# Performance work log

Measured on AMD Instinct MI355X. Metric: run time of the kernel, lower is better.

Reference implementation:

```python
import jax, jax.numpy as jnp
import numpy as np

B, S, V, E, H, NL, DFF = 16, 16, 64, 64, 8, 4, 2048
L = S * V
DH = E // H
NUM_GRIDS = 100
POI_DIM = 8
OV_DIM = 8


def setup_inputs() -> dict:
    key = jax.random.key(0)
    ks = jax.random.split(key, 32)
    sc = 0.05
    inp = {}
    inp['features'] = jax.random.normal(ks[0], (B, S, V, 3), jnp.float32)
    inp['overlap_tag'] = jax.random.randint(ks[1], (B, S, V), 0, 3)
    inp['poi_id'] = jax.random.randint(ks[2], (B, S, V), 0, NUM_GRIDS + 1)
    # embedders
    inp['W_raw'] = jax.random.normal(ks[3], (3, E), jnp.float32) * sc
    inp['b_raw'] = jnp.zeros((E,), jnp.float32)
    inp['pos_tab'] = jax.random.normal(ks[4], (S, E), jnp.float32) * sc
    inp['type_tab'] = jax.random.normal(ks[5], (V, E), jnp.float32) * sc
    inp['poi_tab'] = jax.random.normal(ks[6], (NUM_GRIDS + 1, POI_DIM), jnp.float32) * sc
    inp['overlap_tab'] = jax.random.normal(ks[7], (3, OV_DIM), jnp.float32) * sc
    inp['W_comb'] = jax.random.normal(ks[8], (E + OV_DIM + POI_DIM, E), jnp.float32) * sc
    inp['b_comb'] = jnp.zeros((E,), jnp.float32)
    # transformer layers (stacked over NL)
    inp['Wqkv'] = jax.random.normal(ks[9], (NL, E, 3 * E), jnp.float32) * sc
    inp['bqkv'] = jnp.zeros((NL, 3 * E), jnp.float32)
    inp['Wo'] = jax.random.normal(ks[10], (NL, E, E), jnp.float32) * sc
    inp['bo'] = jnp.zeros((NL, E), jnp.float32)
    inp['ln1_s'] = jnp.ones((NL, E), jnp.float32)
    inp['ln1_b'] = jnp.zeros((NL, E), jnp.float32)
    inp['W1'] = jax.random.normal(ks[11], (NL, E, DFF), jnp.float32) * sc
    inp['b1'] = jnp.zeros((NL, DFF), jnp.float32)
    inp['W2'] = jax.random.normal(ks[12], (NL, DFF, E), jnp.float32) * sc
    inp['b2'] = jnp.zeros((NL, E), jnp.float32)
    inp['ln2_s'] = jnp.ones((NL, E), jnp.float32)
    inp['ln2_b'] = jnp.zeros((NL, E), jnp.float32)
    inp['W_head'] = jax.random.normal(ks[13], (E, 3), jnp.float32) * sc
    inp['b_head'] = jnp.zeros((3,), jnp.float32)
    return inp


def _layer_norm(x, s, b):
    m = x.mean(-1, keepdims=True)
    v = ((x - m) ** 2).mean(-1, keepdims=True)
    return (x - m) / jnp.sqrt(v + 1e-5) * s + b


def _forward(features, overlap_tag, poi_id, W_raw, b_raw, pos_tab, type_tab,
             poi_tab, overlap_tab, W_comb, b_comb, Wqkv, bqkv, Wo, bo,
             ln1_s, ln1_b, W1, b1, W2, b2, ln2_s, ln2_b, W_head, b_head):
    # padding_idx=0 rows are zero (as in nn.Embedding(padding_idx=0))
    poi_tab = poi_tab.at[0].set(0.0)
    overlap_tab = overlap_tab.at[0].set(0.0)

    zero_mask = (features.sum(-1) == 0).reshape(B, L)  # [B, L]
    ov_idx = jnp.maximum(overlap_tag, 0)
    poi_idx = jnp.maximum(poi_id, 0)

    feat_e = features @ W_raw + b_raw                    # [B,S,V,E]
    concat = jnp.concatenate([feat_e, overlap_tab[ov_idx], poi_tab[poi_idx]], axis=-1)
    x = (concat @ W_comb + b_comb).reshape(B, L, E)      # [B,L,E]

    t_idx = jnp.repeat(jnp.arange(S), V)                 # [L]
    v_idx = jnp.tile(jnp.arange(V), S)                   # [L]
    struct_mask = (t_idx[:, None] != t_idx[None, :]) & (v_idx[:, None] != v_idx[None, :])
    full_mask = struct_mask[None] | zero_mask[:, None, :] | zero_mask[:, :, None]  # [B,L,L]
    bias = jnp.where(full_mask, -jnp.inf, 0.0)[:, None, :, :]  # [B,1,L,L]

    x = x + pos_tab[t_idx][None] + type_tab[v_idx][None]

    scale = 1.0 / jnp.sqrt(jnp.asarray(DH, x.dtype))
    for l in range(NL):
        qkv = x @ Wqkv[l] + bqkv[l]                      # [B,L,3E]
        q, k, v = jnp.split(qkv, 3, axis=-1)
        q = q.reshape(B, L, H, DH)
        k = k.reshape(B, L, H, DH)
        v = v.reshape(B, L, H, DH)
        scores = jnp.einsum('bqhd,bkhd->bhqk', q, k) * scale + bias
        attn = jax.nn.softmax(scores, axis=-1)
        o = jnp.einsum('bhqk,bkhd->bqhd', attn, v).reshape(B, L, E)
        x = _layer_norm(x + o @ Wo[l] + bo[l], ln1_s[l], ln1_b[l])
        ff = jax.nn.relu(x @ W1[l] + b1[l]) @ W2[l] + b2[l]
        x = _layer_norm(x + ff, ln2_s[l], ln2_b[l])

    last = x.reshape(B, S, V, E)[:, -1]                  # [B,V,E]
    return last @ W_head + b_head                        # [B,V,3]


def reference(features, overlap_tag, poi_id, W_raw, b_raw, pos_tab, type_tab,
              poi_tab, overlap_tab, W_comb, b_comb, Wqkv, bqkv, Wo, bo,
              ln1_s, ln1_b, W1, b1, W2, b2, ln2_s, ln2_b, W_head, b_head):
    return _forward(features, overlap_tag, poi_id, W_raw, b_raw, pos_tab, type_tab,
                    poi_tab, overlap_tab, W_comb, b_comb, Wqkv, bqkv, Wo, bo,
                    ln1_s, ln1_b, W1, b1, W2, b2, ln2_s, ln2_b, W_head, b_head)
```

## Files before the change

kernel.cpp:

```cpp
#include <hip/hip_runtime.h>
#include <math.h>

#define BB 16
#define SS 16
#define VVV 64
#define EE 64
#define HHH 8
#define NLAYER 4
#define DFF_ 2048
#define LL 1024
#define BL 16384
#define PERL 131072

typedef __attribute__((ext_vector_type(8))) _Float16 half8;
typedef __attribute__((ext_vector_type(4))) _Float16 half4v;
typedef __attribute__((ext_vector_type(2))) _Float16 half2v;
typedef __attribute__((ext_vector_type(4))) float f32x4;

#if defined(__has_builtin)
#if __has_builtin(__builtin_amdgcn_fdot2)
#define HAVE_FDOT2 1
#endif
#endif

#define SW64(m, k)  (((m) << 6) + ((((k) >> 3) ^ ((m) & 7)) << 3) + ((k) & 7))


__global__ __launch_bounds__(256) void k_prep(
    const float* __restrict__ W1, const float* __restrict__ W2,
    const float* __restrict__ Wqkv, const float* __restrict__ Wo,
    const float* __restrict__ Wcomb,
    _Float16* __restrict__ w1f, _Float16* __restrict__ w2f,
    _Float16* __restrict__ wqkvf, _Float16* __restrict__ wof,
    _Float16* __restrict__ wcombt)
{
  __shared__ float t[64 * 65];
  int bx = blockIdx.x;
  int cc = threadIdx.x & 63, rr = threadIdx.x >> 6;

  if (bx >= 272) {
    int r0 = (bx - 272) * 64;
#pragma unroll
    for (int i = 0; i < 16; i++) {
      int r = i * 4 + rr;
      if (r0 + r < 80) t[r * 65 + cc] = Wcomb[(size_t)(r0 + r) * 64 + cc];
    }
    __syncthreads();
#pragma unroll
    for (int i = 0; i < 16; i++) {
      int c = i * 4 + rr;
      if (r0 + c < 80) wcombt[(size_t)cc * 80 + r0 + c] = (_Float16)t[c * 65 + cc];
    }
    return;
  }

  const float* src; _Float16* dst; int astr;
  if (bx < 128) {
    int l = bx >> 5, g = bx & 31;
    src = W1 + (size_t)l * PERL + g * 64; astr = 2048;
    dst = w1f + (size_t)(l * 32 + g) * 4096;
  } else if (bx < 256) {
    int j = bx - 128; int l = j >> 5, g = j & 31;
    src = W2 + (size_t)l * PERL + (size_t)g * 64 * 64; astr = 64;
    dst = w2f + (size_t)(l * 32 + g) * 4096;
  } else if (bx < 268) {
    int j = bx - 256; int l = j / 3, g = j % 3;
    src = Wqkv + (size_t)l * 64 * 192 + g * 64; astr = 192;
    dst = wqkvf + (size_t)(l * 3 + g) * 4096;
  } else {
    int l = bx - 268;
    src = Wo + (size_t)l * 4096; astr = 64;
    dst = wof + (size_t)l * 4096;
  }
#pragma unroll
  for (int i = 0; i < 16; i++) {
    int a = i * 4 + rr;
    t[cc * 65 + a] = src[(size_t)a * astr + cc];
  }
  __syncthreads();
#pragma unroll
  for (int it = 0; it < 2; it++) {
    int c = threadIdx.x + it * 256;
    int frag = c >> 6, lane = c & 63;
    int m = (frag >> 1) * 16 + (lane & 15);
    int k0 = (frag & 1) * 32 + (lane >> 4) * 8;
    const float* tr = &t[m * 65 + k0];
    half8 h;
#pragma unroll
    for (int j = 0; j < 8; j++) h[j] = (_Float16)tr[j];
    *(half8*)&dst[(size_t)c * 8] = h;
  }
}

__device__ __forceinline__ void qkv_nb(
    const half8 (&af)[2][2], const _Float16* __restrict__ wqkvf,
    const float* __restrict__ bqkv, _Float16* __restrict__ qbuf,
    _Float16* __restrict__ kbuf, _Float16* __restrict__ vbuf,
    int bx, int nb, int wm, int wn, int lane)
{
  int quad = lane >> 4, l15 = lane & 15;
  const _Float16* bt = wqkvf + (size_t)nb * 4096;
  half8 bf[2][2];
#pragma unroll
  for (int nt = 0; nt < 2; nt++)
#pragma unroll
    for (int ks = 0; ks < 2; ks++)
      bf[nt][ks] = *(const half8*)&bt[(size_t)(((wn * 2 + nt) * 2 + ks) * 512) +
                                      lane * 8];
  f32x4 acc[2][2];
#pragma unroll
  for (int mt = 0; mt < 2; mt++)
#pragma unroll
    for (int nt = 0; nt < 2; nt++) {
      float bv = bqkv[nb * 64 + wn * 32 + nt * 16 + l15];
      acc[mt][nt] = (f32x4){bv, bv, bv, bv};
    }
#pragma unroll
  for (int ks = 0; ks < 2; ks++)
#pragma unroll
    for (int mt = 0; mt < 2; mt++)
#pragma unroll
      for (int nt = 0; nt < 2; nt++)
        acc[mt][nt] = __builtin_amdgcn_mfma_f32_16x16x32_f16(
            af[mt][ks], bf[nt][ks], acc[mt][nt], 0, 0, 0);
  _Float16* dst = (nb == 0) ? qbuf : ((nb == 1) ? kbuf : vbuf);
#pragma unroll
  for (int mt = 0; mt < 2; mt++)
#pragma unroll
    for (int nt = 0; nt < 2; nt++) {
      int col = wn * 32 + nt * 16 + l15;
      int h = col >> 3, d = col & 7;
#pragma unroll
      for (int r = 0; r < 4; r++) {
        int row = bx * 64 + wm * 32 + mt * 16 + quad * 4 + r;
        int b = row >> 10, rb = row & 1023;
        dst[((size_t)(b * 8 + h) * 1024 + rb) * 8 + d] = (_Float16)acc[mt][nt][r];
      }
    }
}

__device__ __forceinline__ void ffn_load(
    const _Float16* __restrict__ w1f, const _Float16* __restrict__ w2f, int g,
    half8 (&a1)[2][2], half8 (&b2w)[2][2], int wm, int wn, int lane)
{
  const _Float16* w1t_ = w1f + (size_t)g * 4096;
  const _Float16* w2t_ = w2f + (size_t)g * 4096;
#pragma unroll
  for (int ht = 0; ht < 2; ht++)
#pragma unroll
    for (int ks = 0; ks < 2; ks++)
      a1[ht][ks] = *(const half8*)&w1t_[(size_t)(((wm * 2 + ht) * 2 + ks) * 512) +
                                        lane * 8];
#pragma unroll
  for (int nt = 0; nt < 2; nt++)
#pragma unroll
    for (int ks = 0; ks < 2; ks++)
      b2w[nt][ks] = *(const half8*)&w2t_[(size_t)(((wn * 2 + nt) * 2 + ks) * 512) +
                                         lane * 8];
}

__device__ __forceinline__ void ffn_step(
    const half8 (&a1)[2][2], const half8 (&b2w)[2][2], const half8 (&xb)[2][2],
    _Float16* hsbuf, const float* __restrict__ b1, int g, f32x4 (&acc)[2][2],
    int wm, int wn, int lane)
{
  int quad = lane >> 4, l15 = lane & 15;
  f32x4 hacc[2][2];
#pragma unroll
  for (int ht = 0; ht < 2; ht++)
#pragma unroll
    for (int mt = 0; mt < 2; mt++) hacc[ht][mt] = (f32x4){0.f, 0.f, 0.f, 0.f};
#pragma unroll
  for (int ks = 0; ks < 2; ks++)
#pragma unroll
    for (int ht = 0; ht < 2; ht++)
#pragma unroll
      for (int mt = 0; mt < 2; mt++)
        hacc[ht][mt] = __builtin_amdgcn_mfma_f32_16x16x32_f16(
            a1[ht][ks], xb[mt][ks], hacc[ht][mt], 0, 0, 0);
#pragma unroll
  for (int ht = 0; ht < 2; ht++) {
    float4 bb = *(const float4*)&b1[g * 64 + wm * 32 + ht * 16 + quad * 4];
#pragma unroll
    for (int mt = 0; mt < 2; mt++) {
      f32x4 hv = hacc[ht][mt];
      half4v hp = (half4v){
          (_Float16)fmaxf(hv[0] + bb.x, 0.f), (_Float16)fmaxf(hv[1] + bb.y, 0.f),
          (_Float16)fmaxf(hv[2] + bb.z, 0.f), (_Float16)fmaxf(hv[3] + bb.w, 0.f)};
      *(half4v*)&hsbuf[SW64(wn * 32 + mt * 16 + l15,
                            wm * 32 + ht * 16 + quad * 4)] = hp;
    }
  }
  __syncthreads();
#pragma unroll
  for (int ks = 0; ks < 2; ks++)
#pragma unroll
    for (int mt = 0; mt < 2; mt++) {
      half8 a2 = *(const half8*)&hsbuf[SW64(wm * 32 + mt * 16 + l15,
                                            ks * 32 + quad * 8)];
#pragma unroll
      for (int nt = 0; nt < 2; nt++)
        acc[mt][nt] = __builtin_amdgcn_mfma_f32_16x16x32_f16(a2, b2w[nt][ks],
                                                             acc[mt][nt], 0, 0, 0);
    }
}

__global__ __launch_bounds__(256) void k_embqkv(
    const float* __restrict__ features, const int* __restrict__ ovtag,
    const int* __restrict__ poiid, const float* __restrict__ W_raw,
    const float* __restrict__ b_raw, const float* __restrict__ ov_tab,
    const float* __restrict__ poi_tab, const _Float16* __restrict__ wcombt,
    const float* __restrict__ b_comb, const float* __restrict__ pos_tab,
    const float* __restrict__ type_tab, float* __restrict__ x1,
    float* __restrict__ zm, const _Float16* __restrict__ wqkvf,
    const float* __restrict__ bqkv, _Float16* __restrict__ qbuf,
    _Float16* __restrict__ kbuf, _Float16* __restrict__ vbuf)
{
  constexpr int KP = 104;
  __shared__ _Float16 As[64 * KP];
  __shared__ _Float16 Bs[64 * KP];
  __shared__ _Float16 xs[4096];
  int tid = threadIdx.x;
  int bx = blockIdx.x;
  int m0 = bx * 64;
  int wave = tid >> 6, lane = tid & 63, quad = lane >> 4, l15 = lane & 15;
  int wm = wave >> 1, wn = wave & 1;
  for (int p = tid; p < 1536; p += 256) {
    int r = p / 24, s = p - r * 24; int c = s * 4;
    int row = m0 + r;
    float f0 = features[row * 3 + 0];
    float f1 = features[row * 3 + 1];
    float f2 = features[row * 3 + 2];
    if (s == 0) zm[row] = ((f0 + f1 + f2) == 0.f) ? 1.f : 0.f;
    half4v h;
#pragma unroll
    for (int j = 0; j < 4; j++) {
      int cc = c + j; float v;
      if (cc < 64) {
        v = b_raw[cc] + f0 * W_raw[cc] + f1 * W_raw[64 + cc] + f2 * W_raw[128 + cc];
      } else if (cc < 72) {
        int tt = ovtag[row]; v = (tt <= 0) ? 0.f : ov_tab[tt * 8 + cc - 64];
      } else if (cc < 80) {
        int tt = poiid[row]; v = (tt <= 0) ? 0.f : poi_tab[tt * 8 + cc - 72];
      } else v = 0.f;
      h[j] = (_Float16)v;
    }
    *(half4v*)&As[r * KP + c] = h;
  }
  for (int p = tid; p < 1536; p += 256) {
    int r = p / 24, s = p - r * 24; int c = s * 4;
    half4v h = (half4v){0, 0, 0, 0};
    if (c < 80) h = *(const half4v*)&wcombt[r * 80 + c];
    *(half4v*)&Bs[r * KP + c] = h;
  }
  __syncthreads();
  f32x4 acc[2][2];
#pragma unroll
  for (int mt = 0; mt < 2; mt++)
#pragma unroll
    for (int nt = 0; nt < 2; nt++) {
      float bv = b_comb[wn * 32 + nt * 16 + l15];
      acc[mt][nt] = (f32x4){bv, bv, bv, bv};
    }
#pragma unroll
  for (int ks = 0; ks < 3; ks++) {
    half8 af[2], bf[2];
#pragma unroll
    for (int mt = 0; mt < 2; mt++)
      af[mt] = *(const half8*)&As[(wm * 32 + mt * 16 + l15) * KP + ks * 32 + quad * 8];
#pragma unroll
    for (int nt = 0; nt < 2; nt++)
      bf[nt] = *(const half8*)&Bs[(wn * 32 + nt * 16 + l15) * KP + ks * 32 + quad * 8];
#pragma unroll
    for (int mt = 0; mt < 2; mt++)
#pragma unroll
      for (int nt = 0; nt < 2; nt++)
        acc[mt][nt] = __builtin_amdgcn_mfma_f32_16x16x32_f16(af[mt], bf[nt],
                                                             acc[mt][nt], 0, 0, 0);
  }
#pragma unroll
  for (int mt = 0; mt < 2; mt++)
#pragma unroll
    for (int nt = 0; nt < 2; nt++)
#pragma unroll
      for (int r = 0; r < 4; r++) {
        int lrow = wm * 32 + mt * 16 + quad * 4 + r;
        int row = m0 + lrow;
        int col = wn * 32 + nt * 16 + l15;
        int l = row & (LL - 1);
        float v = acc[mt][nt][r] +
            pos_tab[(l >> 6) * 64 + col] + type_tab[(l & 63) * 64 + col];
        x1[(size_t)row * 64 + col] = v;
        xs[SW64(lrow, col)] = (_Float16)v;
      }
  __syncthreads();
  half8 af[2][2];
#pragma unroll
  for (int mt = 0; mt < 2; mt++)
#pragma unroll
    for (int ks = 0; ks < 2; ks++)
      af[mt][ks] = *(const half8*)&xs[SW64(wm * 32 + mt * 16 + l15,
                                           ks * 32 + quad * 8)];
  for (int nb = 0; nb < 3; nb++)
    qkv_nb(af, wqkvf, bqkv, qbuf, kbuf, vbuf, bx, nb, wm, wn, lane);
}

__global__ __launch_bounds__(256) void k_attn2(
    const _Float16* __restrict__ qbuf, const _Float16* __restrict__ kbuf,
    const _Float16* __restrict__ vbuf, const float* __restrict__ zm,
    _Float16* __restrict__ obuf)
{
  __shared__ _Float16 Ks[1024 * 8];
  __shared__ _Float16 Vs[1024 * 8];
  __shared__ float zs[1024];
  int blk = blockIdx.x;
  int qb = blk & 3, h = (blk >> 2) & 7, b = blk >> 5;
  int qrow = qb * 256 + threadIdx.x;
  half8 qh = *(const half8*)&qbuf[(size_t)(b * 8 + h) * 8192 + (size_t)qrow * 8];
  const _Float16* kb = kbuf + (size_t)(b * 8 + h) * 8192;
  const _Float16* vb = vbuf + (size_t)(b * 8 + h) * 8192;
  for (int p = threadIdx.x; p < 1024; p += 256) {
    *(half8*)&Ks[p * 8] = *(const half8*)&kb[p * 8];
    *(half8*)&Vs[p * 8] = *(const half8*)&vb[p * 8];
    zs[p] = zm[b * LL + p];
  }
  __syncthreads();
  int tq = qrow >> 6, vq = qrow & 63;
  const float scale = 0.3535533905932738f;
  float m = -INFINITY, lsum = 0.f;
  float acc[8] = {0.f, 0.f, 0.f, 0.f, 0.f, 0.f, 0.f, 0.f};
  bool zmq = (zs[qrow] != 0.f);

  auto attend = [&](int k) {
    if (zs[k] != 0.f) return;
    half8 kk = *(const half8*)&Ks[k * 8];
    float s = 0.f;
#ifdef HAVE_FDOT2
#pragma unroll
    for (int j = 0; j < 4; j++) {
      half2v qa = (half2v){qh[2 * j], qh[2 * j + 1]};
      half2v ka = (half2v){kk[2 * j], kk[2 * j + 1]};
      s = __builtin_amdgcn_fdot2(qa, ka, s, false);
    }
#else
#pragma unroll
    for (int j = 0; j < 8; j++) s += (float)qh[j] * (float)kk[j];
#endif
    s *= scale;
    half8 vv = *(const half8*)&Vs[k * 8];
    if (s <= m) {
      float p = __expf(s - m);
      lsum += p;
#pragma unroll
      for (int d = 0; d < 8; d++) acc[d] += p * (float)vv[d];
    } else {
      float r = __expf(m - s);
      lsum = lsum * r + 1.f;
#pragma unroll
      for (int d = 0; d < 8; d++) acc[d] = acc[d] * r + (float)vv[d];
      m = s;
    }
  };

  if (!zmq) {
    for (int vv = 0; vv < 64; vv++) attend(tq * 64 + vv);
    for (int tt = 0; tt < 16; tt++) {
      if (tt == tq) continue;
      attend(tt * 64 + vq);
    }
  }
  float inv = 1.f / lsum;
  half8 o;
#pragma unroll
  for (int d = 0; d < 8; d++) o[d] = (_Float16)(acc[d] * inv);
  size_t tile = (size_t)(b * 16 + (qrow >> 6));
  int frag = ((qrow >> 4) & 3) * 2 + (h >> 2);
  int flane = (h & 3) * 16 + (qrow & 15);
  *(half8*)&obuf[tile * 4096 + frag * 512 + flane * 8] = o;
}

__global__ __launch_bounds__(512) void k_layer(
    const _Float16* __restrict__ obuf, const _Float16* __restrict__ wof,
    const float* __restrict__ bo, float* __restrict__ x1,
    const float* __restrict__ ln1_s, const float* __restrict__ ln1_b,
    const _Float16* __restrict__ w1f, const _Float16* __restrict__ w2f,
    const float* __restrict__ b1, const float* __restrict__ b2,
    const float* __restrict__ ln2_s, const float* __restrict__ ln2_b,
    const _Float16* __restrict__ wqkvf, const float* __restrict__ bqkv,
    _Float16* __restrict__ qbuf, _Float16* __restrict__ kbuf,
    _Float16* __restrict__ vbuf, int doqkv,
    const float* __restrict__ Wh, const float* __restrict__ bh,
    float* __restrict__ out)
{
  __shared__ float ots[64 * 68];
  __shared__ _Float16 xs[4096];
  __shared__ float x2f[4096];
  __shared__ _Float16 hs[2][2][4096];
  int tid = threadIdx.x;
  int bx = blockIdx.x;
  int wave = tid >> 6, lane = tid & 63;
  int quad = lane >> 4, l15 = lane & 15;
  int grp = wave >> 2, w4 = wave & 3;
  int wm = w4 >> 1, wn = w4 & 1;

  {
    const _Float16* ot = obuf + (size_t)bx * 4096;
    int mq = grp * 2 + wm;
    half8 af[2], bf[2][2];
#pragma unroll
    for (int ks = 0; ks < 2; ks++)
      af[ks] = *(const half8*)&ot[(size_t)((mq * 2 + ks) * 512) + lane * 8];
#pragma unroll
    for (int nt = 0; nt < 2; nt++)
#pragma unroll
      for (int ks = 0; ks < 2; ks++)
        bf[nt][ks] = *(const half8*)&wof[(size_t)(((wn * 2 + nt) * 2 + ks) * 512) +
                                         lane * 8];
    f32x4 acc[2];
#pragma unroll
    for (int nt = 0; nt < 2; nt++) {
      float bv = bo[wn * 32 + nt * 16 + l15];
      acc[nt] = (f32x4){bv, bv, bv, bv};
    }
#pragma unroll
    for (int ks = 0; ks < 2; ks++)
#pragma unroll
      for (int nt = 0; nt < 2; nt++)
        acc[nt] = __builtin_amdgcn_mfma_f32_16x16x32_f16(af[ks], bf[nt][ks],
                                                         acc[nt], 0, 0, 0);
#pragma unroll
    for (int nt = 0; nt < 2; nt++)
#pragma unroll
      for (int r = 0; r < 4; r++)
        ots[(mq * 16 + quad * 4 + r) * 68 + wn * 32 + nt * 16 + l15] = acc[nt][r];
  }
  __syncthreads();
  for (int i = 0; i < 8; i++) {
    int row = wave * 8 + i;
    size_t off = (size_t)(bx * 64 + row) * 64 + lane;
    float val = ots[row * 68 + lane] + x1[off];
    float sum = val;
#pragma unroll
    for (int o = 32; o > 0; o >>= 1) sum += __shfl_xor(sum, o);
    float mean = sum * (1.f / 64.f);
    float d = val - mean;
    float sq = d * d;
#pragma unroll
    for (int o = 32; o > 0; o >>= 1) sq += __shfl_xor(sq, o);
    float xv = d * rsqrtf(sq * (1.f / 64.f) + 1e-5f) * ln1_s[lane] + ln1_b[lane];
    x2f[row * 64 + lane] = xv;
    xs[SW64(row, lane)] = (_Float16)xv;
  }
  __syncthreads();

  half8 xb[2][2];
#pragma unroll
  for (int mt = 0; mt < 2; mt++)
#pragma unroll
    for (int ks = 0; ks < 2; ks++)
      xb[mt][ks] = *(const half8*)&xs[SW64(wn * 32 + mt * 16 + l15,
                                           ks * 32 + quad * 8)];
  f32x4 acc[2][2];
#pragma unroll
  for (int mt = 0; mt < 2; mt++)
#pragma unroll
    for (int nt = 0; nt < 2; nt++) {
      float bv = (grp == 0) ? b2[wn * 32 + nt * 16 + l15] : 0.f;
      acc[mt][nt] = (f32x4){bv, bv, bv, bv};
    }
  half8 a1x[2][2], b2x[2][2], a1y[2][2], b2y[2][2];
  ffn_load(w1f, w2f, grp, a1x, b2x, wm, wn, lane);
  for (int ii = 0; ii < 8; ii++) {
    ffn_load(w1f, w2f, ii * 4 + 2 + grp, a1y, b2y, wm, wn, lane);
    ffn_step(a1x, b2x, xb, &hs[grp][0][0], b1, ii * 4 + grp, acc, wm, wn, lane);
    if (ii < 7) ffn_load(w1f, w2f, ii * 4 + 4 + grp, a1x, b2x, wm, wn, lane);
    ffn_step(a1y, b2y, xb, &hs[grp][1][0], b1, ii * 4 + 2 + grp, acc, wm, wn, lane);
  }
  __syncthreads();
  if (grp == 0) {
#pragma unroll
    for (int mt = 0; mt < 2; mt++)
#pragma unroll
      for (int nt = 0; nt < 2; nt++)
#pragma unroll
        for (int r = 0; r < 4; r++)
          ots[(wm * 32 + mt * 16 + quad * 4 + r) * 68 + wn * 32 + nt * 16 + l15] =
              acc[mt][nt][r];
  }
  __syncthreads();
  if (grp == 1) {
#pragma unroll
    for (int mt = 0; mt < 2; mt++)
#pragma unroll
      for (int nt = 0; nt < 2; nt++)
#pragma unroll
        for (int r = 0; r < 4; r++)
          ots[(wm * 32 + mt * 16 + quad * 4 + r) * 68 + wn * 32 + nt * 16 + l15] +=
              acc[mt][nt][r];
  }
  __syncthreads();
  for (int i = 0; i < 8; i++) {
    int row = wave * 8 + i;
    size_t off = (size_t)(bx * 64 + row) * 64 + lane;
    float val = ots[row * 68 + lane] + x2f[row * 64 + lane];
    float sum = val;
#pragma unroll
    for (int o = 32; o > 0; o >>= 1) sum += __shfl_xor(sum, o);
    float mean = sum * (1.f / 64.f);
    float d = val - mean;
    float sq = d * d;
#pragma unroll
    for (int o = 32; o > 0; o >>= 1) sq += __shfl_xor(sq, o);
    float xv = d * rsqrtf(sq * (1.f / 64.f) + 1e-5f) * ln2_s[lane] + ln2_b[lane];
    x1[off] = xv;
    x2f[row * 64 + lane] = xv;
    xs[SW64(row, lane)] = (_Float16)xv;
  }
  if (!doqkv) {
    __syncthreads();
    if ((bx & 15) == 15 && tid < 192) {
      int b = bx >> 4;
      int v = tid / 3, j = tid - v * 3;
      float a = bh[j];
      for (int e = 0; e < 64; e++)
        a += x2f[v * 64 + e] * Wh[e * 3 + j];
      out[((size_t)(b * 64 + v)) * 3 + j] = a;
    }
    return;
  }
  __syncthreads();
  half8 af[2][2];
#pragma unroll
  for (int mt = 0; mt < 2; mt++)
#pragma unroll
    for (int ks = 0; ks < 2; ks++)
      af[mt][ks] = *(const half8*)&xs[SW64(wm * 32 + mt * 16 + l15,
                                           ks * 32 + quad * 8)];
  for (int nb = grp; nb < 3; nb += 2)
    qkv_nb(af, wqkvf, bqkv, qbuf, kbuf, vbuf, bx, nb, wm, wn, lane);
}

extern "C" void kernel_launch(void* const* d_in, const int* in_sizes, int n_in,
                              void* d_out, int out_size, void* d_ws, size_t ws_size,
                              hipStream_t stream) {
  const float* features = (const float*)d_in[0];
  const int*   ovtag    = (const int*)d_in[1];
  const int*   poiid    = (const int*)d_in[2];
  const float* W_raw    = (const float*)d_in[3];
  const float* b_raw    = (const float*)d_in[4];
  const float* pos_tab  = (const float*)d_in[5];
  const float* type_tab = (const float*)d_in[6];
  const float* poi_tab  = (const float*)d_in[7];
  const float* ov_tab   = (const float*)d_in[8];
  const float* W_comb   = (const float*)d_in[9];
  const float* b_comb   = (const float*)d_in[10];
  const float* Wqkv     = (const float*)d_in[11];
  const float* bqkv     = (const float*)d_in[12];
  const float* Wo       = (const float*)d_in[13];
  const float* bo       = (const float*)d_in[14];
  const float* ln1_s    = (const float*)d_in[15];
  const float* ln1_b    = (const float*)d_in[16];
  const float* W1       = (const float*)d_in[17];
  const float* b1       = (const float*)d_in[18];
  const float* W2       = (const float*)d_in[19];
  const float* b2       = (const float*)d_in[20];
  const float* ln2_s    = (const float*)d_in[21];
  const float* ln2_b    = (const float*)d_in[22];
  const float* W_head   = (const float*)d_in[23];
  const float* b_head   = (const float*)d_in[24];
  float* out = (float*)d_out;
  float* ws  = (float*)d_ws;

  float* zm  = ws;
  float* x1  = zm + BL;
  _Float16* qbuf   = (_Float16*)(x1 + (size_t)BL * 64);
  _Float16* kbuf   = qbuf + (size_t)BL * 64;
  _Float16* vbuf   = kbuf + (size_t)BL * 64;
  _Float16* obuf16 = vbuf + (size_t)BL * 64;
  _Float16* wcombt = obuf16 + (size_t)BL * 64;
  _Float16* w1f    = wcombt + 5120;
  _Float16* w2f    = w1f + (size_t)NLAYER * PERL;
  _Float16* wqkvf  = w2f + (size_t)NLAYER * PERL;
  _Float16* wof    = wqkvf + (size_t)NLAYER * 3 * 4096;

  k_prep<<<274, 256, 0, stream>>>(W1, W2, Wqkv, Wo, W_comb,
                                  w1f, w2f, wqkvf, wof, wcombt);
  k_embqkv<<<256, 256, 0, stream>>>(features, ovtag, poiid, W_raw, b_raw,
                                    ov_tab, poi_tab, wcombt, b_comb,
                                    pos_tab, type_tab, x1, zm,
                                    wqkvf, bqkv, qbuf, kbuf, vbuf);
  for (int l = 0; l < NLAYER; l++) {
    k_attn2<<<512, 256, 0, stream>>>(qbuf, kbuf, vbuf, zm, obuf16);
    int doqkv = (l < NLAYER - 1);
    k_layer<<<256, 512, 0, stream>>>(
        obuf16, wof + (size_t)l * 4096, bo + l * EE, x1,
        ln1_s + l * EE, ln1_b + l * EE,
        w1f + (size_t)l * PERL, w2f + (size_t)l * PERL,
        b1 + l * DFF_, b2 + l * EE,
        ln2_s + l * EE, ln2_b + l * EE,
        wqkvf + (size_t)(l + 1 < NLAYER ? l + 1 : 0) * 3 * 4096,
        bqkv + (l + 1 < NLAYER ? l + 1 : 0) * 192,
        qbuf, kbuf, vbuf, doqkv, W_head, b_head, out);
  }
}
```

Before: 317.4 us.

## Fuse attention into per-layer kernel with double-buffered K/V across layers

Removes the separate attention kernel and folds the sparse (same-timestep plus same-variable) attention into the layer kernel. Each block computes attention output for its own 64-row tile across all 8 heads into LDS and feeds it directly to the Wo matmul. This drops a launch per layer and the global round trip of the attention output. Because other blocks still read this layer's K/V while the next layer's K/V are being written, K/V are now ping-ponged between two buffer sets. The online softmax is reworked to process keys in groups of 4 with an additive mask. The trade-off is that K/V are read straight from global memory instead of being staged in LDS, and the grid has fewer threads doing attention.

```diff
diff --git a/kernel.cpp b/kernel.cpp
--- a/kernel.cpp
+++ b/kernel.cpp
@@ -25,6 +25,22 @@
 
 #define SW64(m, k)  (((m) << 6) + ((((k) >> 3) ^ ((m) & 7)) << 3) + ((k) & 7))
 
+
+__device__ __forceinline__ float dot8(half8 a, half8 b) {
+  float s = 0.f;
+#ifdef HAVE_FDOT2
+#pragma unroll
+  for (int j = 0; j < 4; j++) {
+    half2v x = (half2v){a[2 * j], a[2 * j + 1]};
+    half2v y = (half2v){b[2 * j], b[2 * j + 1]};
+    s = __builtin_amdgcn_fdot2(x, y, s, false);
+  }
+#else
+#pragma unroll
+  for (int j = 0; j < 8; j++) s += (float)a[j] * (float)b[j];
+#endif
+  return s;
+}
 
 __global__ __launch_bounds__(256) void k_prep(
     const float* __restrict__ W1, const float* __restrict__ W2,
@@ -95,7 +111,7 @@
 __device__ __forceinline__ void qkv_nb(
     const half8 (&af)[2][2], const _Float16* __restrict__ wqkvf,
     const float* __restrict__ bqkv, _Float16* __restrict__ qbuf,
-    _Float16* __restrict__ kbuf, _Float16* __restrict__ vbuf,
+    _Float16* __restrict__ kvbuf, int set,
     int bx, int nb, int wm, int wn, int lane)
 {
   int quad = lane >> 4, l15 = lane & 15;
@@ -123,7 +139,9 @@
       for (int nt = 0; nt < 2; nt++)
         acc[mt][nt] = __builtin_amdgcn_mfma_f32_16x16x32_f16(
             af[mt][ks], bf[nt][ks], acc[mt][nt], 0, 0, 0);
-  _Float16* dst = (nb == 0) ? qbuf : ((nb == 1) ? kbuf : vbuf);
+  _Float16* dst = (nb == 0)
+      ? qbuf
+      : kvbuf + ((size_t)((set * 2 + nb - 1) * (BB * 8))) * 8192;
 #pragma unroll
   for (int mt = 0; mt < 2; mt++)
 #pragma unroll
@@ -136,72 +154,6 @@
         int b = row >> 10, rb = row & 1023;
         dst[((size_t)(b * 8 + h) * 1024 + rb) * 8 + d] = (_Float16)acc[mt][nt][r];
       }
-    }
-}
-
-__device__ __forceinline__ void ffn_load(
-    const _Float16* __restrict__ w1f, const _Float16* __restrict__ w2f, int g,
-    half8 (&a1)[2][2], half8 (&b2w)[2][2], int wm, int wn, int lane)
-{
-  const _Float16* w1t_ = w1f + (size_t)g * 4096;
-  const _Float16* w2t_ = w2f + (size_t)g * 4096;
-#pragma unroll
-  for (int ht = 0; ht < 2; ht++)
-#pragma unroll
-    for (int ks = 0; ks < 2; ks++)
-      a1[ht][ks] = *(const half8*)&w1t_[(size_t)(((wm * 2 + ht) * 2 + ks) * 512) +
-                                        lane * 8];
-#pragma unroll
-  for (int nt = 0; nt < 2; nt++)
-#pragma unroll
-    for (int ks = 0; ks < 2; ks++)
-      b2w[nt][ks] = *(const half8*)&w2t_[(size_t)(((wn * 2 + nt) * 2 + ks) * 512) +
-                                         lane * 8];
-}
-
-__device__ __forceinline__ void ffn_step(
-    const half8 (&a1)[2][2], const half8 (&b2w)[2][2], const half8 (&xb)[2][2],
-    _Float16* hsbuf, const float* __restrict__ b1, int g, f32x4 (&acc)[2][2],
-    int wm, int wn, int lane)
-{
-  int quad = lane >> 4, l15 = lane & 15;
-  f32x4 hacc[2][2];
-#pragma unroll
-  for (int ht = 0; ht < 2; ht++)
-#pragma unroll
-    for (int mt = 0; mt < 2; mt++) hacc[ht][mt] = (f32x4){0.f, 0.f, 0.f, 0.f};
-#pragma unroll
-  for (int ks = 0; ks < 2; ks++)
-#pragma unroll
-    for (int ht = 0; ht < 2; ht++)
-#pragma unroll
-      for (int mt = 0; mt < 2; mt++)
-        hacc[ht][mt] = __builtin_amdgcn_mfma_f32_16x16x32_f16(
-            a1[ht][ks], xb[mt][ks], hacc[ht][mt], 0, 0, 0);
-#pragma unroll
-  for (int ht = 0; ht < 2; ht++) {
-    float4 bb = *(const float4*)&b1[g * 64 + wm * 32 + ht * 16 + quad * 4];
-#pragma unroll
-    for (int mt = 0; mt < 2; mt++) {
-      f32x4 hv = hacc[ht][mt];
-      half4v hp = (half4v){
-          (_Float16)fmaxf(hv[0] + bb.x, 0.f), (_Float16)fmaxf(hv[1] + bb.y, 0.f),
-          (_Float16)fmaxf(hv[2] + bb.z, 0.f), (_Float16)fmaxf(hv[3] + bb.w, 0.f)};
-      *(half4v*)&hsbuf[SW64(wn * 32 + mt * 16 + l15,
-                            wm * 32 + ht * 16 + quad * 4)] = hp;
-    }
-  }
-  __syncthreads();
-#pragma unroll
-  for (int ks = 0; ks < 2; ks++)
-#pragma unroll
-    for (int mt = 0; mt < 2; mt++) {
-      half8 a2 = *(const half8*)&hsbuf[SW64(wm * 32 + mt * 16 + l15,
-                                            ks * 32 + quad * 8)];
-#pragma unroll
-      for (int nt = 0; nt < 2; nt++)
-        acc[mt][nt] = __builtin_amdgcn_mfma_f32_16x16x32_f16(a2, b2w[nt][ks],
-                                                             acc[mt][nt], 0, 0, 0);
     }
 }
 
@@ -214,7 +166,7 @@
     const float* __restrict__ type_tab, float* __restrict__ x1,
     float* __restrict__ zm, const _Float16* __restrict__ wqkvf,
     const float* __restrict__ bqkv, _Float16* __restrict__ qbuf,
-    _Float16* __restrict__ kbuf, _Float16* __restrict__ vbuf)
+    _Float16* __restrict__ kvbuf)
 {
   constexpr int KP = 104;
   __shared__ _Float16 As[64 * KP];
@@ -302,120 +254,111 @@
       af[mt][ks] = *(const half8*)&xs[SW64(wm * 32 + mt * 16 + l15,
                                            ks * 32 + quad * 8)];
   for (int nb = 0; nb < 3; nb++)
-    qkv_nb(af, wqkvf, bqkv, qbuf, kbuf, vbuf, bx, nb, wm, wn, lane);
+    qkv_nb(af, wqkvf, bqkv, qbuf, kvbuf, 0, bx, nb, wm, wn, lane);
 }
 
-__global__ __launch_bounds__(256) void k_attn2(
-    const _Float16* __restrict__ qbuf, const _Float16* __restrict__ kbuf,
-    const _Float16* __restrict__ vbuf, const float* __restrict__ zm,
-    _Float16* __restrict__ obuf)
-{
-  __shared__ _Float16 Ks[1024 * 8];
-  __shared__ _Float16 Vs[1024 * 8];
-  __shared__ float zs[1024];
-  int blk = blockIdx.x;
-  int qb = blk & 3, h = (blk >> 2) & 7, b = blk >> 5;
-  int qrow = qb * 256 + threadIdx.x;
-  half8 qh = *(const half8*)&qbuf[(size_t)(b * 8 + h) * 8192 + (size_t)qrow * 8];
-  const _Float16* kb = kbuf + (size_t)(b * 8 + h) * 8192;
-  const _Float16* vb = vbuf + (size_t)(b * 8 + h) * 8192;
-  for (int p = threadIdx.x; p < 1024; p += 256) {
-    *(half8*)&Ks[p * 8] = *(const half8*)&kb[p * 8];
-    *(half8*)&Vs[p * 8] = *(const half8*)&vb[p * 8];
-    zs[p] = zm[b * LL + p];
-  }
-  __syncthreads();
-  int tq = qrow >> 6, vq = qrow & 63;
-  const float scale = 0.3535533905932738f;
-  float m = -INFINITY, lsum = 0.f;
-  float acc[8] = {0.f, 0.f, 0.f, 0.f, 0.f, 0.f, 0.f, 0.f};
-  bool zmq = (zs[qrow] != 0.f);
-
-  auto attend = [&](int k) {
-    if (zs[k] != 0.f) return;
-    half8 kk = *(const half8*)&Ks[k * 8];
-    float s = 0.f;
-#ifdef HAVE_FDOT2
-#pragma unroll
-    for (int j = 0; j < 4; j++) {
-      half2v qa = (half2v){qh[2 * j], qh[2 * j + 1]};
-      half2v ka = (half2v){kk[2 * j], kk[2 * j + 1]};
-      s = __builtin_amdgcn_fdot2(qa, ka, s, false);
-    }
-#else
-#pragma unroll
-    for (int j = 0; j < 8; j++) s += (float)qh[j] * (float)kk[j];
-#endif
-    s *= scale;
-    half8 vv = *(const half8*)&Vs[k * 8];
-    if (s <= m) {
-      float p = __expf(s - m);
-      lsum += p;
-#pragma unroll
-      for (int d = 0; d < 8; d++) acc[d] += p * (float)vv[d];
-    } else {
-      float r = __expf(m - s);
-      lsum = lsum * r + 1.f;
-#pragma unroll
-      for (int d = 0; d < 8; d++) acc[d] = acc[d] * r + (float)vv[d];
-      m = s;
-    }
-  };
-
-  if (!zmq) {
-    for (int vv = 0; vv < 64; vv++) attend(tq * 64 + vv);
-    for (int tt = 0; tt < 16; tt++) {
-      if (tt == tq) continue;
-      attend(tt * 64 + vq);
-    }
-  }
-  float inv = 1.f / lsum;
-  half8 o;
-#pragma unroll
-  for (int d = 0; d < 8; d++) o[d] = (_Float16)(acc[d] * inv);
-  size_t tile = (size_t)(b * 16 + (qrow >> 6));
-  int frag = ((qrow >> 4) & 3) * 2 + (h >> 2);
-  int flane = (h & 3) * 16 + (qrow & 15);
-  *(half8*)&obuf[tile * 4096 + frag * 512 + flane * 8] = o;
-}
-
-__global__ __launch_bounds__(512) void k_layer(
-    const _Float16* __restrict__ obuf, const _Float16* __restrict__ wof,
-    const float* __restrict__ bo, float* __restrict__ x1,
+__global__ __launch_bounds__(512, 4) void k_layer3(
+    const _Float16* __restrict__ qbuf, _Float16* __restrict__ kvbuf, int l,
+    const _Float16* __restrict__ wof, const float* __restrict__ bo,
+    float* __restrict__ x1,
     const float* __restrict__ ln1_s, const float* __restrict__ ln1_b,
     const _Float16* __restrict__ w1f, const _Float16* __restrict__ w2f,
     const float* __restrict__ b1, const float* __restrict__ b2,
     const float* __restrict__ ln2_s, const float* __restrict__ ln2_b,
     const _Float16* __restrict__ wqkvf, const float* __restrict__ bqkv,
-    _Float16* __restrict__ qbuf, _Float16* __restrict__ kbuf,
-    _Float16* __restrict__ vbuf, int doqkv,
+    _Float16* __restrict__ qout, int doqkv,
     const float* __restrict__ Wh, const float* __restrict__ bh,
-    float* __restrict__ out)
+    float* __restrict__ out, const float* __restrict__ zm)
 {
-  __shared__ float ots[64 * 68];
+  __shared__ float    xf[4096];
   __shared__ _Float16 xs[4096];
-  __shared__ float x2f[4096];
-  __shared__ _Float16 hs[2][2][4096];
-  int tid = threadIdx.x;
-  int bx = blockIdx.x;
+  __shared__ _Float16 qlds[4096];
+  __shared__ float    zb[1024];
+  __shared__ __align__(16) float smem_u[8192];
+  _Float16* hsu = (_Float16*)smem_u;
+  float* ots = smem_u;
+
+  int tid = threadIdx.x, bx = blockIdx.x;
   int wave = tid >> 6, lane = tid & 63;
   int quad = lane >> 4, l15 = lane & 15;
-  int grp = wave >> 2, w4 = wave & 3;
-  int wm = w4 >> 1, wn = w4 & 1;
-
+  int b = bx >> 4, tq = bx & 15;
+
+  for (int p = tid; p < 1024; p += 512)
+    zb[p] = (zm[b * LL + p] != 0.f) ? -1e30f : 0.f;
+  __syncthreads();
   {
-    const _Float16* ot = obuf + (size_t)bx * 4096;
-    int mq = grp * 2 + wm;
-    half8 af[2], bf[2][2];
-#pragma unroll
-    for (int ks = 0; ks < 2; ks++)
-      af[ks] = *(const half8*)&ot[(size_t)((mq * 2 + ks) * 512) + lane * 8];
-#pragma unroll
-    for (int nt = 0; nt < 2; nt++)
-#pragma unroll
-      for (int ks = 0; ks < 2; ks++)
-        bf[nt][ks] = *(const half8*)&wof[(size_t)(((wn * 2 + nt) * 2 + ks) * 512) +
-                                         lane * 8];
+    int h = wave;
+    half8 qh = *(const half8*)&qbuf[((size_t)(b * 8 + h) * 1024 +
+                                     tq * 64 + lane) * 8];
+    const _Float16* kb = kvbuf + ((size_t)((((l & 1) * 2 + 0) * (BB * 8)) +
+                                           b * 8 + h)) * 8192;
+    const _Float16* vb = kvbuf + ((size_t)((((l & 1) * 2 + 1) * (BB * 8)) +
+                                           b * 8 + h)) * 8192;
+    const float scale = 0.3535533905932738f;
+    float m = -INFINITY, lsum = 0.f;
+    float acc[8] = {0.f, 0.f, 0.f, 0.f, 0.f, 0.f, 0.f, 0.f};
+    bool zmq = (zb[tq * 64 + lane] < -1.f);
+    if (!zmq) {
+      for (int g = 0; g < 16; g++) {
+        half8 kk[4], vv[4]; float s[4];
+#pragma unroll
+        for (int j = 0; j < 4; j++) {
+          int k = tq * 64 + g * 4 + j;
+          kk[j] = *(const half8*)&kb[k * 8];
+          vv[j] = *(const half8*)&vb[k * 8];
+        }
+#pragma unroll
+        for (int j = 0; j < 4; j++)
+          s[j] = dot8(qh, kk[j]) * scale + zb[tq * 64 + g * 4 + j];
+        float gm = fmaxf(fmaxf(s[0], s[1]), fmaxf(s[2], s[3]));
+        float nm = fmaxf(m, gm);
+        float r = __expf(m - nm);
+        float p0 = __expf(s[0] - nm), p1 = __expf(s[1] - nm);
+        float p2 = __expf(s[2] - nm), p3 = __expf(s[3] - nm);
+        lsum = lsum * r + (p0 + p1) + (p2 + p3);
+#pragma unroll
+        for (int d = 0; d < 8; d++)
+          acc[d] = acc[d] * r + p0 * (float)vv[0][d] + p1 * (float)vv[1][d] +
+                   p2 * (float)vv[2][d] + p3 * (float)vv[3][d];
+        m = nm;
+      }
+      for (int g = 0; g < 4; g++) {
+        half8 kk[4], vv[4]; float s[4];
+#pragma unroll
+        for (int j = 0; j < 4; j++) {
+          int tt = g * 4 + j;
+          int k = tt * 64 + lane;
+          kk[j] = *(const half8*)&kb[k * 8];
+          vv[j] = *(const half8*)&vb[k * 8];
+          s[j] = (tt == tq) ? -1e30f : zb[k];
+        }
+#pragma unroll
+        for (int j = 0; j < 4; j++)
+          s[j] += dot8(qh, kk[j]) * scale;
+        float gm = fmaxf(fmaxf(s[0], s[1]), fmaxf(s[2], s[3]));
+        float nm = fmaxf(m, gm);
+        float r = __expf(m - nm);
+        float p0 = __expf(s[0] - nm), p1 = __expf(s[1] - nm);
+        float p2 = __expf(s[2] - nm), p3 = __expf(s[3] - nm);
+        lsum = lsum * r + (p0 + p1) + (p2 + p3);
+#pragma unroll
+        for (int d = 0; d < 8; d++)
+          acc[d] = acc[d] * r + p0 * (float)vv[0][d] + p1 * (float)vv[1][d] +
+                   p2 * (float)vv[2][d] + p3 * (float)vv[3][d];
+        m = nm;
+      }
+    }
+    float inv = 1.f / lsum;
+    half8 o;
+#pragma unroll
+    for (int d = 0; d < 8; d++) o[d] = (_Float16)(acc[d] * inv);
+    int frag = (lane >> 4) * 2 + (h >> 2);
+    int fl = (h & 3) * 16 + (lane & 15);
+    *(half8*)&qlds[frag * 512 + fl * 8] = o;
+  }
+  __syncthreads();
+  {
+    int wm = wave >> 1, wn = wave & 1;
     f32x4 acc[2];
 #pragma unroll
     for (int nt = 0; nt < 2; nt++) {
@@ -423,16 +366,20 @@
       acc[nt] = (f32x4){bv, bv, bv, bv};
     }
 #pragma unroll
-    for (int ks = 0; ks < 2; ks++)
-#pragma unroll
-      for (int nt = 0; nt < 2; nt++)
-        acc[nt] = __builtin_amdgcn_mfma_f32_16x16x32_f16(af[ks], bf[nt][ks],
-                                                         acc[nt], 0, 0, 0);
+    for (int ks = 0; ks < 2; ks++) {
+      half8 af = *(const half8*)&qlds[(wm * 2 + ks) * 512 + lane * 8];
+#pragma unroll
+      for (int nt = 0; nt < 2; nt++) {
+        half8 bf = *(const half8*)&wof[(size_t)(((wn * 2 + nt) * 2 + ks) * 512) +
+                                       lane * 8];
+        acc[nt] = __builtin_amdgcn_mfma_f32_16x16x32_f16(af, bf, acc[nt], 0, 0, 0);
+      }
+    }
 #pragma unroll
     for (int nt = 0; nt < 2; nt++)
 #pragma unroll
       for (int r = 0; r < 4; r++)
-        ots[(mq * 16 + quad * 4 + r) * 68 + wn * 32 + nt * 16 + l15] = acc[nt][r];
+        ots[(wm * 16 + quad * 4 + r) * 68 + wn * 32 + nt * 16 + l15] = acc[nt][r];
   }
   __syncthreads();
   for (int i = 0; i < 8; i++) {
@@ -448,61 +395,123 @@
 #pragma unroll
     for (int o = 32; o > 0; o >>= 1) sq += __shfl_xor(sq, o);
     float xv = d * rsqrtf(sq * (1.f / 64.f) + 1e-5f) * ln1_s[lane] + ln1_b[lane];
-    x2f[row * 64 + lane] = xv;
+    xf[row * 64 + lane] = xv;
     xs[SW64(row, lane)] = (_Float16)xv;
   }
   __syncthreads();
-
-  half8 xb[2][2];
-#pragma unroll
-  for (int mt = 0; mt < 2; mt++)
-#pragma unroll
-    for (int ks = 0; ks < 2; ks++)
-      xb[mt][ks] = *(const half8*)&xs[SW64(wn * 32 + mt * 16 + l15,
-                                           ks * 32 + quad * 8)];
-  f32x4 acc[2][2];
-#pragma unroll
-  for (int mt = 0; mt < 2; mt++)
-#pragma unroll
-    for (int nt = 0; nt < 2; nt++) {
-      float bv = (grp == 0) ? b2[wn * 32 + nt * 16 + l15] : 0.f;
-      acc[mt][nt] = (f32x4){bv, bv, bv, bv};
-    }
-  half8 a1x[2][2], b2x[2][2], a1y[2][2], b2y[2][2];
-  ffn_load(w1f, w2f, grp, a1x, b2x, wm, wn, lane);
-  for (int ii = 0; ii < 8; ii++) {
-    ffn_load(w1f, w2f, ii * 4 + 2 + grp, a1y, b2y, wm, wn, lane);
-    ffn_step(a1x, b2x, xb, &hs[grp][0][0], b1, ii * 4 + grp, acc, wm, wn, lane);
-    if (ii < 7) ffn_load(w1f, w2f, ii * 4 + 4 + grp, a1x, b2x, wm, wn, lane);
-    ffn_step(a1y, b2y, xb, &hs[grp][1][0], b1, ii * 4 + 2 + grp, acc, wm, wn, lane);
-  }
-  __syncthreads();
-  if (grp == 0) {
+  {
+    int grp = wave >> 2, w4 = wave & 3;
+    int wm = w4 >> 1, wn = w4 & 1;
+    half8 xb[2][2];
 #pragma unroll
     for (int mt = 0; mt < 2; mt++)
 #pragma unroll
+      for (int ks = 0; ks < 2; ks++)
+        xb[mt][ks] = *(const half8*)&xs[SW64(wn * 32 + mt * 16 + l15,
+                                             ks * 32 + quad * 8)];
+    f32x4 acc[2][2];
+#pragma unroll
+    for (int mt = 0; mt < 2; mt++)
+#pragma unroll
+      for (int nt = 0; nt < 2; nt++) {
+        float bv = (grp == 0) ? b2[wn * 32 + nt * 16 + l15] : 0.f;
+        acc[mt][nt] = (f32x4){bv, bv, bv, bv};
+      }
+    half8 a1x[2][2], b2x[2][2], a1y[2][2], b2y[2][2];
+    auto loadw = [&](int g, half8 (&a1)[2][2], half8 (&b2w)[2][2]) {
+      const _Float16* w1t_ = w1f + (size_t)g * 4096;
+      const _Float16* w2t_ = w2f + (size_t)g * 4096;
+#pragma unroll
+      for (int ht = 0; ht < 2; ht++)
+#pragma unroll
+        for (int ks = 0; ks < 2; ks++)
+          a1[ht][ks] = *(const half8*)&w1t_[(size_t)(((wm * 2 + ht) * 2 + ks) * 512)
+                                            + lane * 8];
+#pragma unroll
       for (int nt = 0; nt < 2; nt++)
 #pragma unroll
-        for (int r = 0; r < 4; r++)
-          ots[(wm * 32 + mt * 16 + quad * 4 + r) * 68 + wn * 32 + nt * 16 + l15] =
-              acc[mt][nt][r];
-  }
-  __syncthreads();
-  if (grp == 1) {
-#pragma unroll
-    for (int mt = 0; mt < 2; mt++)
-#pragma unroll
-      for (int nt = 0; nt < 2; nt++)
-#pragma unroll
-        for (int r = 0; r < 4; r++)
-          ots[(wm * 32 + mt * 16 + quad * 4 + r) * 68 + wn * 32 + nt * 16 + l15] +=
-              acc[mt][nt][r];
+        for (int ks = 0; ks < 2; ks++)
+          b2w[nt][ks] = *(const half8*)&w2t_[(size_t)(((wn * 2 + nt) * 2 + ks) * 512)
+                                             + lane * 8];
+    };
+    auto step = [&](const half8 (&a1)[2][2], const half8 (&b2w)[2][2],
+                    _Float16* hsbuf, int g) {
+      f32x4 hacc[2][2];
+#pragma unroll
+      for (int ht = 0; ht < 2; ht++)
+#pragma unroll
+        for (int mt = 0; mt < 2; mt++) hacc[ht][mt] = (f32x4){0.f, 0.f, 0.f, 0.f};
+#pragma unroll
+      for (int ks = 0; ks < 2; ks++)
+#pragma unroll
+        for (int ht = 0; ht < 2; ht++)
+#pragma unroll
+          for (int mt = 0; mt < 2; mt++)
+            hacc[ht][mt] = __builtin_amdgcn_mfma_f32_16x16x32_f16(
+                a1[ht][ks], xb[mt][ks], hacc[ht][mt], 0, 0, 0);
+#pragma unroll
+      for (int ht = 0; ht < 2; ht++) {
+        float4 bb = *(const float4*)&b1[g * 64 + wm * 32 + ht * 16 + quad * 4];
+#pragma unroll
+        for (int mt = 0; mt < 2; mt++) {
+          f32x4 hv = hacc[ht][mt];
+          half4v hp = (half4v){
+              (_Float16)fmaxf(hv[0] + bb.x, 0.f),
+              (_Float16)fmaxf(hv[1] + bb.y, 0.f),
+              (_Float16)fmaxf(hv[2] + bb.z, 0.f),
+              (_Float16)fmaxf(hv[3] + bb.w, 0.f)};
+          *(half4v*)&hsbuf[SW64(wn * 32 + mt * 16 + l15,
+                                wm * 32 + ht * 16 + quad * 4)] = hp;
+        }
+      }
+      __syncthreads();
+#pragma unroll
+      for (int ks = 0; ks < 2; ks++)
+#pragma unroll
+        for (int mt = 0; mt < 2; mt++) {
+          half8 a2 = *(const half8*)&hsbuf[SW64(wm * 32 + mt * 16 + l15,
+                                                ks * 32 + quad * 8)];
+#pragma unroll
+          for (int nt = 0; nt < 2; nt++)
+            acc[mt][nt] = __builtin_amdgcn_mfma_f32_16x16x32_f16(
+                a2, b2w[nt][ks], acc[mt][nt], 0, 0, 0);
+        }
+    };
+    loadw(grp, a1x, b2x);
+    for (int ii = 0; ii < 8; ii++) {
+      loadw(ii * 4 + 2 + grp, a1y, b2y);
+      step(a1x, b2x, &hsu[(grp * 2 + 0) * 4096], ii * 4 + grp);
+      if (ii < 7) loadw(ii * 4 + 4 + grp, a1x, b2x);
+      step(a1y, b2y, &hsu[(grp * 2 + 1) * 4096], ii * 4 + 2 + grp);
+    }
+    __syncthreads();
+    if (grp == 0) {
+#pragma unroll
+      for (int mt = 0; mt < 2; mt++)
+#pragma unroll
+        for (int nt = 0; nt < 2; nt++)
+#pragma unroll
+          for (int r = 0; r < 4; r++)
+            ots[(wm * 32 + mt * 16 + quad * 4 + r) * 68 + wn * 32 + nt * 16 + l15]
+                = acc[mt][nt][r];
+    }
+    __syncthreads();
+    if (grp == 1) {
+#pragma unroll
+      for (int mt = 0; mt < 2; mt++)
+#pragma unroll
+        for (int nt = 0; nt < 2; nt++)
+#pragma unroll
+          for (int r = 0; r < 4; r++)
+            ots[(wm * 32 + mt * 16 + quad * 4 + r) * 68 + wn * 32 + nt * 16 + l15]
+                += acc[mt][nt][r];
+    }
   }
   __syncthreads();
   for (int i = 0; i < 8; i++) {
     int row = wave * 8 + i;
     size_t off = (size_t)(bx * 64 + row) * 64 + lane;
-    float val = ots[row * 68 + lane] + x2f[row * 64 + lane];
+    float val = ots[row * 68 + lane] + xf[row * 64 + lane];
     float sum = val;
 #pragma unroll
     for (int o = 32; o > 0; o >>= 1) sum += __shfl_xor(sum, o);
@@ -513,31 +522,30 @@
     for (int o = 32; o > 0; o >>= 1) sq += __shfl_xor(sq, o);
     float xv = d * rsqrtf(sq * (1.f / 64.f) + 1e-5f) * ln2_s[lane] + ln2_b[lane];
     x1[off] = xv;
-    x2f[row * 64 + lane] = xv;
+    xf[row * 64 + lane] = xv;
     xs[SW64(row, lane)] = (_Float16)xv;
   }
-  if (!doqkv) {
-    __syncthreads();
-    if ((bx & 15) == 15 && tid < 192) {
-      int b = bx >> 4;
+  __syncthreads();
+  if (doqkv) {
+    int grp = wave >> 2, w4 = wave & 3;
+    int wm = w4 >> 1, wn = w4 & 1;
+    half8 af[2][2];
+#pragma unroll
+    for (int mt = 0; mt < 2; mt++)
+#pragma unroll
+      for (int ks = 0; ks < 2; ks++)
+        af[mt][ks] = *(const half8*)&xs[SW64(wm * 32 + mt * 16 + l15,
+                                             ks * 32 + quad * 8)];
+    for (int nb = grp; nb < 3; nb += 2)
+      qkv_nb(af, wqkvf, bqkv, qout, kvbuf, (l + 1) & 1, bx, nb, wm, wn, lane);
+  } else {
+    if (tq == 15 && tid < 192) {
       int v = tid / 3, j = tid - v * 3;
       float a = bh[j];
-      for (int e = 0; e < 64; e++)
-        a += x2f[v * 64 + e] * Wh[e * 3 + j];
+      for (int e = 0; e < 64; e++) a += xf[v * 64 + e] * Wh[e * 3 + j];
       out[((size_t)(b * 64 + v)) * 3 + j] = a;
     }
-    return;
-  }
-  __syncthreads();
-  half8 af[2][2];
-#pragma unroll
-  for (int mt = 0; mt < 2; mt++)
-#pragma unroll
-    for (int ks = 0; ks < 2; ks++)
-      af[mt][ks] = *(const half8*)&xs[SW64(wm * 32 + mt * 16 + l15,
-                                           ks * 32 + quad * 8)];
-  for (int nb = grp; nb < 3; nb += 2)
-    qkv_nb(af, wqkvf, bqkv, qbuf, kbuf, vbuf, bx, nb, wm, wn, lane);
+  }
 }
 
 extern "C" void kernel_launch(void* const* d_in, const int* in_sizes, int n_in,
@@ -571,13 +579,11 @@
   float* out = (float*)d_out;
   float* ws  = (float*)d_ws;
 
-  float* zm  = ws;
-  float* x1  = zm + BL;
+  float* zm = ws;
+  float* x1 = zm + BL;
   _Float16* qbuf   = (_Float16*)(x1 + (size_t)BL * 64);
-  _Float16* kbuf   = qbuf + (size_t)BL * 64;
-  _Float16* vbuf   = kbuf + (size_t)BL * 64;
-  _Float16* obuf16 = vbuf + (size_t)BL * 64;
-  _Float16* wcombt = obuf16 + (size_t)BL * 64;
+  _Float16* kvbuf  = qbuf + (size_t)BL * 64;
+  _Float16* wcombt = kvbuf + 4 * (size_t)BL * 64;
   _Float16* w1f    = wcombt + 5120;
   _Float16* w2f    = w1f + (size_t)NLAYER * PERL;
   _Float16* wqkvf  = w2f + (size_t)NLAYER * PERL;
@@ -588,18 +594,18 @@
   k_embqkv<<<256, 256, 0, stream>>>(features, ovtag, poiid, W_raw, b_raw,
                                     ov_tab, poi_tab, wcombt, b_comb,
                                     pos_tab, type_tab, x1, zm,
-                                    wqkvf, bqkv, qbuf, kbuf, vbuf);
+                                    wqkvf, bqkv, qbuf, kvbuf);
   for (int l = 0; l < NLAYER; l++) {
-    k_attn2<<<512, 256, 0, stream>>>(qbuf, kbuf, vbuf, zm, obuf16);
     int doqkv = (l < NLAYER - 1);
-    k_layer<<<256, 512, 0, stream>>>(
-        obuf16, wof + (size_t)l * 4096, bo + l * EE, x1,
+    k_layer3<<<256, 512, 0, stream>>>(
+        qbuf, kvbuf, l,
+        wof + (size_t)l * 4096, bo + l * EE, x1,
         ln1_s + l * EE, ln1_b + l * EE,
         w1f + (size_t)l * PERL, w2f + (size_t)l * PERL,
         b1 + l * DFF_, b2 + l * EE,
         ln2_s + l * EE, ln2_b + l * EE,
         wqkvf + (size_t)(l + 1 < NLAYER ? l + 1 : 0) * 3 * 4096,
         bqkv + (l + 1 < NLAYER ? l + 1 : 0) * 192,
-        qbuf, kbuf, vbuf, doqkv, W_head, b_head, out);
+        qbuf, doqkv, W_head, b_head, out, zm);
   }
 }
```

After: 340.2 us. 1.07x slower.
